# Optimization experiments

Hardware: AMD Instinct MI355X
Metric: run time of the kernel (lower is better)

Reference implementation:

```python
import jax, jax.numpy as jnp
import numpy as np

DIM = 512
HEADS = 8
DIM_HEAD = 64
HIDDEN = HEADS * DIM_HEAD  # 512
SCALE = DIM_HEAD ** -0.5


def setup_inputs() -> dict:
    key = jax.random.key(0)
    k1, k2, k3, k4 = jax.random.split(key, 4)
    B, N = 8, 4096
    x = jax.random.normal(k1, (B, DIM, N), dtype=jnp.float32)
    # Conv1d with kernel_size=1, no bias -> weight [out, in]
    w_qkv = jax.random.normal(k2, (HIDDEN * 3, DIM), dtype=jnp.float32) * (DIM ** -0.5)
    w_out = jax.random.normal(k3, (DIM, HIDDEN), dtype=jnp.float32) * (HIDDEN ** -0.5)
    b_out = jax.random.normal(k4, (DIM,), dtype=jnp.float32) * 0.01
    return {"x": x, "w_qkv": w_qkv, "w_out": w_out, "b_out": b_out}


def reference(x, w_qkv, w_out, b_out):
    B, _, N = x.shape
    # pointwise conv1d == channel GEMM: [3*hidden, dim] x [b, dim, n]
    qkv = jnp.einsum('oi,bin->bon', w_qkv, x)
    q, k, v = jnp.split(qkv, 3, axis=1)
    # b (h c) n -> b h c n
    reshape = lambda t: t.reshape(B, HEADS, DIM_HEAD, N)
    q, k, v = reshape(q), reshape(k), reshape(v)
    q = q * SCALE
    k = jax.nn.softmax(k, axis=-1)  # softmax over sequence dim n
    # context: [b h d e] = sum_n k[b h d n] v[b h e n]
    context = jnp.einsum('bhdn,bhen->bhde', k, v)
    # out: [b h e n] = sum_d context[b h d e] q[b h d n]
    out = jnp.einsum('bhde,bhdn->bhen', context, q)
    out = out.reshape(B, HIDDEN, N)  # b (h e) n
    return jnp.einsum('oi,bin->bon', w_out, out) + b_out[None, :, None]
```

## Files before the change

kernel.cpp:

```cpp
#include <hip/hip_runtime.h>
#include <hip/hip_bf16.h>
#include <cstdint>

typedef unsigned short u16;
typedef __attribute__((ext_vector_type(8))) short bf16x8;
typedef __attribute__((ext_vector_type(4))) float f32x4;

__device__ __forceinline__ u16 f2b(float f) {
  union { float f; unsigned u; } x; x.f = f;
  unsigned r = x.u + 0x7fffu + ((x.u >> 16) & 1u);
  return (u16)(r >> 16);
}
__device__ __forceinline__ float b2f(u16 u) {
  union { unsigned u; float f; } x; x.u = ((unsigned)u) << 16;
  return x.f;
}
__device__ __forceinline__ void gld16(void* lds, const void* g) {
  __builtin_amdgcn_global_load_lds((const __attribute__((address_space(1))) void*)g,
                                   (__attribute__((address_space(3))) void*)lds, 16, 0, 0);
}
__device__ __forceinline__ int sw_idx(int n, int c) {
  return n * 64 + ((((c >> 2) ^ (n >> 2)) & 15) << 2) + (c & 3);
}
__device__ __forceinline__ int ekb(int row, int c2) {
  return (row * 256 + c2) ^ ((((row >> 3) ^ row) & 7) << 4);
}

__global__ __launch_bounds__(256) void prep(const float* __restrict__ w_qkv,
                                            u16* __restrict__ wkvh,
                                            u16* __restrict__ wqT,
                                            float* __restrict__ zbuf) {
  const int tid = threadIdx.x;
  const int blk = blockIdx.x;
  if (blk < 512) {
    const int i = blk * 1024 + tid * 4;
    const int ri = i >> 9;
    const int col = i & 511;
    const int h = (ri >> 6) & 7;
    const int orow = h * 128 + ((ri >> 9) << 6) + (ri & 63);
    const float4 v = *(const float4*)(w_qkv + 262144 + i);
    ushort4 r; r.x = f2b(v.x); r.y = f2b(v.y); r.z = f2b(v.z); r.w = f2b(v.w);
    *(ushort4*)(wkvh + orow * 512 + col) = r;
  } else if (blk < 576) {
    __shared__ u16 t[4096];
    const int bb = blk - 512;
    const int i0 = (bb & 7) * 64;
    const int c0 = (bb >> 3) * 64;
    const int il = (tid & 15) * 4;
    const int cl = tid >> 4;
#pragma unroll
    for (int r = 0; r < 4; r++) {
      const int c = cl + r * 16;
      const float4 v = *(const float4*)(w_qkv + (c0 + c) * 512 + i0 + il);
      t[sw_idx(il + 0, c)] = f2b(v.x);
      t[sw_idx(il + 1, c)] = f2b(v.y);
      t[sw_idx(il + 2, c)] = f2b(v.z);
      t[sw_idx(il + 3, c)] = f2b(v.w);
    }
    __syncthreads();
    const int cw = (tid & 15) * 4;
#pragma unroll
    for (int r = 0; r < 4; r++) {
      const int i = cl + r * 16;
      const u16* tp = &t[sw_idx(i, cw)];
      ushort4 o; o.x = tp[0]; o.y = tp[1]; o.z = tp[2]; o.w = tp[3];
      *(ushort4*)(wqT + (i0 + i) * 512 + c0 + cw) = o;
    }
  } else {
    const int zi = (blk - 576) * 1024 + tid * 4;
    if (zi < 266240) *(float4*)(zbuf + zi) = float4{0.f, 0.f, 0.f, 0.f};
  }
}

__global__ __launch_bounds__(256) void xt_kern(const float* __restrict__ x,
                                               u16* __restrict__ xt) {
  __shared__ u16 t[4096];
  const int tid = threadIdx.x;
  const int b = blockIdx.z;
  const int n0 = blockIdx.x * 64;
  const int c0 = blockIdx.y * 64;
  const int nl = (tid & 15) * 4;
  const int cl = tid >> 4;
#pragma unroll
  for (int r = 0; r < 4; r++) {
    const int c = cl + r * 16;
    const float4 v = *(const float4*)(x + ((long)b * 512 + c0 + c) * 4096 + n0 + nl);
    t[sw_idx(nl + 0, c)] = f2b(v.x);
    t[sw_idx(nl + 1, c)] = f2b(v.y);
    t[sw_idx(nl + 2, c)] = f2b(v.z);
    t[sw_idx(nl + 3, c)] = f2b(v.w);
  }
  __syncthreads();
  const int cw = (tid & 15) * 4;
#pragma unroll
  for (int r = 0; r < 4; r++) {
    const int n = cl + r * 16;
    const u16* tp = &t[sw_idx(n, cw)];
    ushort4 o; o.x = tp[0]; o.y = tp[1]; o.z = tp[2]; o.w = tp[3];
    *(ushort4*)(xt + ((long)b * 4096 + n0 + n) * 512 + c0 + cw) = o;
  }
}

__global__ __launch_bounds__(256, 4) void kvctx(const u16* __restrict__ wkvh,
                                                const u16* __restrict__ xt,
                                                float* __restrict__ ctx,
                                                float* __restrict__ rsum) {
  __shared__ u16 sh[16384];
  u16* As = sh;
  u16* Bs = sh + 4096;
  u16* Ek = sh;
  u16* Vs = sh + 8192;

  const int tid = threadIdx.x;
  const int wid = tid >> 6;
  const int lane = tid & 63;
  const int wm = wid >> 1, wn = wid & 1;

  const int flat = blockIdx.x;
  const int xcd = flat & 7;
  const int slot = flat >> 3;
  const int h = slot & 7;
  const int tile = xcd * 32 + (slot >> 3);
  const int nc = tile & 31;
  const int b = tile >> 5;
  const int bh = b * 8 + h;

  const u16* Ab = wkvh + (long)h * 128 * 512;
  const u16* Bb = xt + ((long)b * 4096 + (long)nc * 128) * 512;
  const int q8 = (lane >> 4) * 8;
  const int mr = lane & 15;
  const int quad = lane >> 4;

  f32x4 acc[4][4] = {};

  for (int kk = 0; kk < 512; kk += 32) {
    __syncthreads();
#pragma unroll
    for (int i = 0; i < 2; i++) {
      const int slot2 = i * 256 + tid;
      const int row = slot2 >> 2;
      const int kc = (slot2 & 3) * 8;
      gld16((char*)As + i * 4096 + wid * 1024, Ab + (long)row * 512 + kk + kc);
      gld16((char*)Bs + i * 4096 + wid * 1024, Bb + (long)row * 512 + kk + kc);
    }
    __syncthreads();
    bf16x8 af[4], bfv[4];
#pragma unroll
    for (int i = 0; i < 4; i++)
      af[i] = *(const bf16x8*)(As + (wm * 64 + i * 16 + mr) * 32 + q8);
#pragma unroll
    for (int j = 0; j < 4; j++)
      bfv[j] = *(const bf16x8*)(Bs + (wn * 64 + j * 16 + mr) * 32 + q8);
#pragma unroll
    for (int i = 0; i < 4; i++)
#pragma unroll
      for (int j = 0; j < 4; j++)
        acc[i][j] = __builtin_amdgcn_mfma_f32_16x16x32_bf16(af[i], bfv[j], acc[i][j], 0, 0, 0);
  }

  __syncthreads();
  u16* dst = (wm == 0) ? Ek : Vs;
#pragma unroll
  for (int i = 0; i < 4; i++) {
#pragma unroll
    for (int r = 0; r < 4; r++) {
      const int row = i * 16 + quad * 4 + r;
      float sloc = 0.f;
#pragma unroll
      for (int j = 0; j < 4; j++) {
        float v = acc[i][j][r];
        if (wm == 0) v = __expf(v);
        const u16 bv = f2b(v);
        const int col = wn * 64 + j * 16 + mr;
        *(u16*)((char*)dst + ekb(row, col * 2)) = bv;
        if (wm == 0) sloc += b2f(bv);
      }
      if (wm == 0) {
        sloc += __shfl_xor(sloc, 1);
        sloc += __shfl_xor(sloc, 2);
        sloc += __shfl_xor(sloc, 4);
        sloc += __shfl_xor(sloc, 8);
        if (mr == 0) atomicAdd(rsum + (long)bh * 64 + row, sloc);
      }
    }
  }
  __syncthreads();

  f32x4 acc2[2][2] = {};
#pragma unroll
  for (int ks = 0; ks < 4; ks++) {
    bf16x8 ef[2], vf[2];
#pragma unroll
    for (int ii = 0; ii < 2; ii++) {
      const int row = wm * 32 + ii * 16 + mr;
      ef[ii] = *(const bf16x8*)((const char*)Ek + ekb(row, (ks * 32 + q8) * 2));
    }
#pragma unroll
    for (int jj = 0; jj < 2; jj++) {
      const int row = wn * 32 + jj * 16 + mr;
      vf[jj] = *(const bf16x8*)((const char*)Vs + ekb(row, (ks * 32 + q8) * 2));
    }
#pragma unroll
    for (int ii = 0; ii < 2; ii++)
#pragma unroll
      for (int jj = 0; jj < 2; jj++)
        acc2[ii][jj] = __builtin_amdgcn_mfma_f32_16x16x32_bf16(ef[ii], vf[jj], acc2[ii][jj], 0, 0, 0);
  }

  float* cb = ctx + (long)bh * 4096;
#pragma unroll
  for (int ii = 0; ii < 2; ii++)
#pragma unroll
    for (int jj = 0; jj < 2; jj++)
#pragma unroll
      for (int r = 0; r < 4; r++) {
        const int d = wm * 32 + ii * 16 + quad * 4 + r;
        const int e = wn * 32 + jj * 16 + mr;
        atomicAdd(cb + d * 64 + e, acc2[ii][jj][r]);
      }
}

__global__ __launch_bounds__(256) void wc_kern(const float* __restrict__ ctxp,
                                               const float* __restrict__ rsump,
                                               const float* __restrict__ wout,
                                               u16* __restrict__ Wc) {
  __shared__ float cs[64 * 65];
  const int tid = threadIdx.x;
  const int bh = blockIdx.x, og = blockIdx.y;
  const int b = bh >> 3, h = bh & 7;
  for (int i = tid; i < 4096; i += 256) {
    const int d = i >> 6, e = i & 63;
    cs[e * 65 + d] = ctxp[(long)bh * 4096 + i] / rsump[(long)bh * 64 + d];
  }
  __syncthreads();
  const int d = tid & 63;
  const int o0 = og * 128 + (tid >> 6) * 32;
  float csr[64];
#pragma unroll
  for (int e = 0; e < 64; e++) csr[e] = cs[e * 65 + d];
  u16* wcp = Wc + (long)b * 512 * 512;
  for (int rr = 0; rr < 32; rr++) {
    const int o = o0 + rr;
    const float* wrow = wout + (long)o * 512 + h * 64;
    float a0 = 0.f, a1 = 0.f, a2 = 0.f, a3 = 0.f;
#pragma unroll
    for (int e = 0; e < 64; e += 4) {
      a0 += wrow[e + 0] * csr[e + 0];
      a1 += wrow[e + 1] * csr[e + 1];
      a2 += wrow[e + 2] * csr[e + 2];
      a3 += wrow[e + 3] * csr[e + 3];
    }
    wcp[(long)o * 512 + h * 64 + d] = f2b((a0 + a1) + (a2 + a3));
  }
}

__global__ __launch_bounds__(256) void weff_gemm(const u16* __restrict__ Wc,
                                                 const u16* __restrict__ wqT,
                                                 u16* __restrict__ Weff) {
  __shared__ u16 As[128 * 32];
  __shared__ u16 Bs[128 * 32];
  const int tid = threadIdx.x;
  const int wid = tid >> 6;
  const int lane = tid & 63;
  const int wm = wid >> 1, wn = wid & 1;
  const int gn = blockIdx.x, gm = blockIdx.y, b = blockIdx.z;

  const u16* Ab = Wc + (long)b * 512 * 512 + (long)gm * 128 * 512;
  const u16* Bb = wqT + (long)gn * 128 * 512;

  f32x4 acc[4][4] = {};
  const int q8 = (lane >> 4) * 8;
  const int mr = lane & 15;

  for (int kk = 0; kk < 512; kk += 32) {
    __syncthreads();
#pragma unroll
    for (int i = 0; i < 2; i++) {
      const int slot = i * 256 + tid;
      const int row = slot >> 2;
      const int kc = (slot & 3) * 8;
      gld16((char*)As + i * 4096 + wid * 1024, Ab + (long)row * 512 + kk + kc);
      gld16((char*)Bs + i * 4096 + wid * 1024, Bb + (long)row * 512 + kk + kc);
    }
    __syncthreads();
    bf16x8 af[4], bfv[4];
#pragma unroll
    for (int i = 0; i < 4; i++)
      af[i] = *(const bf16x8*)(As + (wm * 64 + i * 16 + mr) * 32 + q8);
#pragma unroll
    for (int j = 0; j < 4; j++)
      bfv[j] = *(const bf16x8*)(Bs + (wn * 64 + j * 16 + mr) * 32 + q8);
#pragma unroll
    for (int i = 0; i < 4; i++)
#pragma unroll
      for (int j = 0; j < 4; j++)
        acc[i][j] = __builtin_amdgcn_mfma_f32_16x16x32_bf16(af[i], bfv[j], acc[i][j], 0, 0, 0);
  }

  const int col = lane & 15;
  const int quad = lane >> 4;
  u16* wb = Weff + (long)b * 512 * 512;
#pragma unroll
  for (int i = 0; i < 4; i++)
#pragma unroll
    for (int r = 0; r < 4; r++) {
      const int grow = gm * 128 + wm * 64 + i * 16 + quad * 4 + r;
#pragma unroll
      for (int j = 0; j < 4; j++) {
        const int gcol = gn * 128 + wn * 64 + j * 16 + col;
        wb[(long)grow * 512 + gcol] = f2b(acc[i][j][r] * 0.125f);
      }
    }
}

__global__ __launch_bounds__(256) void out_gemm(const u16* __restrict__ Weff,
                                                const u16* __restrict__ xt,
                                                const float* __restrict__ bias,
                                                float* __restrict__ outp) {
  __shared__ u16 As[128 * 32];
  __shared__ u16 Bs[128 * 32];
  const int tid = threadIdx.x;
  const int wid = tid >> 6;
  const int lane = tid & 63;
  const int wm = wid >> 1, wn = wid & 1;
  const int gn = blockIdx.x, gm = blockIdx.y, b = blockIdx.z;

  const u16* Ab = Weff + (long)b * 512 * 512 + (long)gm * 128 * 512;
  const u16* Bb = xt + ((long)b * 4096 + (long)gn * 128) * 512;

  f32x4 acc[4][4] = {};
  const int q8 = (lane >> 4) * 8;
  const int mr = lane & 15;

  for (int kk = 0; kk < 512; kk += 32) {
    __syncthreads();
#pragma unroll
    for (int i = 0; i < 2; i++) {
      const int slot = i * 256 + tid;
      const int row = slot >> 2;
      const int kc = (slot & 3) * 8;
      gld16((char*)As + i * 4096 + wid * 1024, Ab + (long)row * 512 + kk + kc);
      gld16((char*)Bs + i * 4096 + wid * 1024, Bb + (long)row * 512 + kk + kc);
    }
    __syncthreads();
    bf16x8 af[4], bfv[4];
#pragma unroll
    for (int i = 0; i < 4; i++)
      af[i] = *(const bf16x8*)(As + (wm * 64 + i * 16 + mr) * 32 + q8);
#pragma unroll
    for (int j = 0; j < 4; j++)
      bfv[j] = *(const bf16x8*)(Bs + (wn * 64 + j * 16 + mr) * 32 + q8);
#pragma unroll
    for (int i = 0; i < 4; i++)
#pragma unroll
      for (int j = 0; j < 4; j++)
        acc[i][j] = __builtin_amdgcn_mfma_f32_16x16x32_bf16(af[i], bfv[j], acc[i][j], 0, 0, 0);
  }

  const int col = lane & 15;
  const int quad = lane >> 4;
#pragma unroll
  for (int i = 0; i < 4; i++)
#pragma unroll
    for (int r = 0; r < 4; r++) {
      const int grow = gm * 128 + wm * 64 + i * 16 + quad * 4 + r;
      const float bv = bias[grow];
#pragma unroll
      for (int j = 0; j < 4; j++) {
        const long gcol = (long)gn * 128 + wn * 64 + j * 16 + col;
        outp[((long)b * 512 + grow) * 4096 + gcol] = acc[i][j][r] + bv;
      }
    }
}

extern "C" void kernel_launch(void* const* d_in, const int* in_sizes, int n_in,
                              void* d_out, int out_size, void* d_ws, size_t ws_size,
                              hipStream_t stream) {
  const float* x = (const float*)d_in[0];
  const float* w_qkv = (const float*)d_in[1];
  const float* w_out = (const float*)d_in[2];
  const float* b_out = (const float*)d_in[3];
  float* out = (float*)d_out;
  char* ws = (char*)d_ws;

  u16* xt = (u16*)(ws + 0);
  u16* wkvh = (u16*)(ws + 33554432);
  u16* wqT = (u16*)(ws + 34603008);
  u16* wc = (u16*)(ws + 35127296);
  u16* weff = (u16*)(ws + 39321600);
  float* ctx = (float*)(ws + 43515904);
  float* rsum = (float*)(ws + 44564480);

  prep<<<836, 256, 0, stream>>>(w_qkv, wkvh, wqT, ctx);
  xt_kern<<<dim3(64, 8, 8), 256, 0, stream>>>(x, xt);
  kvctx<<<2048, 256, 0, stream>>>(wkvh, xt, ctx, rsum);
  wc_kern<<<dim3(64, 4), 256, 0, stream>>>(ctx, rsum, w_out, wc);
  weff_gemm<<<dim3(4, 4, 8), 256, 0, stream>>>(wc, wqT, weff);
  out_gemm<<<dim3(32, 4, 8), 256, 0, stream>>>(weff, xt, b_out, out);
}
```

Before: 265.2 us.

## Double-buffer LDS with XOR swizzle in GEMMs and merge prep kernels

The kvctx and out_gemm main loops now use two LDS buffers. The next K-slice's global_load_lds is issued before computing on the current one, so each step needs one barrier instead of two. The LDS column chunks are XOR-swizzled by row so the fragment reads hit fewer bank conflicts. The x transpose kernel is also folded into the weight prep kernel, removing one launch. The cost is double the LDS per block in out_gemm, which may limit occupancy.

```diff
diff --git a/kernel.cpp b/kernel.cpp
--- a/kernel.cpp
+++ b/kernel.cpp
@@ -26,14 +26,44 @@
   return (row * 256 + c2) ^ ((((row >> 3) ^ row) & 7) << 4);
 }
 
-__global__ __launch_bounds__(256) void prep(const float* __restrict__ w_qkv,
-                                            u16* __restrict__ wkvh,
-                                            u16* __restrict__ wqT,
-                                            float* __restrict__ zbuf) {
+__global__ __launch_bounds__(256) void pre(const float* __restrict__ x,
+                                           u16* __restrict__ xt,
+                                           const float* __restrict__ w_qkv,
+                                           u16* __restrict__ wkvh,
+                                           u16* __restrict__ wqT,
+                                           float* __restrict__ zbuf) {
+  __shared__ u16 t[4096];
   const int tid = threadIdx.x;
   const int blk = blockIdx.x;
-  if (blk < 512) {
-    const int i = blk * 1024 + tid * 4;
+  if (blk < 4096) {
+    const int b = blk >> 9;
+    const int c0 = ((blk >> 6) & 7) * 64;
+    const int n0 = (blk & 63) * 64;
+    const int nl = (tid & 15) * 4;
+    const int cl = tid >> 4;
+#pragma unroll
+    for (int r = 0; r < 4; r++) {
+      const int c = cl + r * 16;
+      const float4 v = *(const float4*)(x + ((long)b * 512 + c0 + c) * 4096 + n0 + nl);
+      t[sw_idx(nl + 0, c)] = f2b(v.x);
+      t[sw_idx(nl + 1, c)] = f2b(v.y);
+      t[sw_idx(nl + 2, c)] = f2b(v.z);
+      t[sw_idx(nl + 3, c)] = f2b(v.w);
+    }
+    __syncthreads();
+    const int cw = (tid & 15) * 4;
+#pragma unroll
+    for (int r = 0; r < 4; r++) {
+      const int n = cl + r * 16;
+      const u16* tp = &t[sw_idx(n, cw)];
+      ushort4 o; o.x = tp[0]; o.y = tp[1]; o.z = tp[2]; o.w = tp[3];
+      *(ushort4*)(xt + ((long)b * 4096 + n0 + n) * 512 + c0 + cw) = o;
+    }
+    return;
+  }
+  const int pblk = blk - 4096;
+  if (pblk < 512) {
+    const int i = pblk * 1024 + tid * 4;
     const int ri = i >> 9;
     const int col = i & 511;
     const int h = (ri >> 6) & 7;
@@ -41,9 +71,8 @@
     const float4 v = *(const float4*)(w_qkv + 262144 + i);
     ushort4 r; r.x = f2b(v.x); r.y = f2b(v.y); r.z = f2b(v.z); r.w = f2b(v.w);
     *(ushort4*)(wkvh + orow * 512 + col) = r;
-  } else if (blk < 576) {
-    __shared__ u16 t[4096];
-    const int bb = blk - 512;
+  } else if (pblk < 576) {
+    const int bb = pblk - 512;
     const int i0 = (bb & 7) * 64;
     const int c0 = (bb >> 3) * 64;
     const int il = (tid & 15) * 4;
@@ -67,37 +96,8 @@
       *(ushort4*)(wqT + (i0 + i) * 512 + c0 + cw) = o;
     }
   } else {
-    const int zi = (blk - 576) * 1024 + tid * 4;
+    const int zi = (pblk - 576) * 1024 + tid * 4;
     if (zi < 266240) *(float4*)(zbuf + zi) = float4{0.f, 0.f, 0.f, 0.f};
-  }
-}
-
-__global__ __launch_bounds__(256) void xt_kern(const float* __restrict__ x,
-                                               u16* __restrict__ xt) {
-  __shared__ u16 t[4096];
-  const int tid = threadIdx.x;
-  const int b = blockIdx.z;
-  const int n0 = blockIdx.x * 64;
-  const int c0 = blockIdx.y * 64;
-  const int nl = (tid & 15) * 4;
-  const int cl = tid >> 4;
-#pragma unroll
-  for (int r = 0; r < 4; r++) {
-    const int c = cl + r * 16;
-    const float4 v = *(const float4*)(x + ((long)b * 512 + c0 + c) * 4096 + n0 + nl);
-    t[sw_idx(nl + 0, c)] = f2b(v.x);
-    t[sw_idx(nl + 1, c)] = f2b(v.y);
-    t[sw_idx(nl + 2, c)] = f2b(v.z);
-    t[sw_idx(nl + 3, c)] = f2b(v.w);
-  }
-  __syncthreads();
-  const int cw = (tid & 15) * 4;
-#pragma unroll
-  for (int r = 0; r < 4; r++) {
-    const int n = cl + r * 16;
-    const u16* tp = &t[sw_idx(n, cw)];
-    ushort4 o; o.x = tp[0]; o.y = tp[1]; o.z = tp[2]; o.w = tp[3];
-    *(ushort4*)(xt + ((long)b * 4096 + n0 + n) * 512 + c0 + cw) = o;
   }
 }
 
@@ -106,8 +106,6 @@
                                                 float* __restrict__ ctx,
                                                 float* __restrict__ rsum) {
   __shared__ u16 sh[16384];
-  u16* As = sh;
-  u16* Bs = sh + 4096;
   u16* Ek = sh;
   u16* Vs = sh + 8192;
 
@@ -127,30 +125,38 @@
 
   const u16* Ab = wkvh + (long)h * 128 * 512;
   const u16* Bb = xt + ((long)b * 4096 + (long)nc * 128) * 512;
-  const int q8 = (lane >> 4) * 8;
   const int mr = lane & 15;
   const int quad = lane >> 4;
+  const int q8 = quad * 8;
+  const int cidx = (quad ^ ((mr >> 1) & 3)) * 8;
 
   f32x4 acc[4][4] = {};
 
-  for (int kk = 0; kk < 512; kk += 32) {
-    __syncthreads();
+  auto stage = [&](int buf, int kk) {
 #pragma unroll
     for (int i = 0; i < 2; i++) {
-      const int slot2 = i * 256 + tid;
-      const int row = slot2 >> 2;
-      const int kc = (slot2 & 3) * 8;
-      gld16((char*)As + i * 4096 + wid * 1024, Ab + (long)row * 512 + kk + kc);
-      gld16((char*)Bs + i * 4096 + wid * 1024, Bb + (long)row * 512 + kk + kc);
-    }
-    __syncthreads();
+      const int s2 = i * 256 + tid;
+      const int row = s2 >> 2;
+      const int kc = (((s2 & 3) ^ ((row >> 1) & 3)) * 8);
+      char* dA = (char*)sh + buf * 16384 + i * 4096 + wid * 1024;
+      gld16(dA, Ab + (long)row * 512 + kk + kc);
+      gld16(dA + 8192, Bb + (long)row * 512 + kk + kc);
+    }
+  };
+
+  stage(0, 0);
+  for (int t = 0; t < 16; t++) {
+    __syncthreads();
+    if (t < 15) stage((t + 1) & 1, (t + 1) * 32);
+    const u16* As = sh + (t & 1) * 8192;
+    const u16* Bs = As + 4096;
     bf16x8 af[4], bfv[4];
 #pragma unroll
     for (int i = 0; i < 4; i++)
-      af[i] = *(const bf16x8*)(As + (wm * 64 + i * 16 + mr) * 32 + q8);
+      af[i] = *(const bf16x8*)(As + (wm * 64 + i * 16 + mr) * 32 + cidx);
 #pragma unroll
     for (int j = 0; j < 4; j++)
-      bfv[j] = *(const bf16x8*)(Bs + (wn * 64 + j * 16 + mr) * 32 + q8);
+      bfv[j] = *(const bf16x8*)(Bs + (wn * 64 + j * 16 + mr) * 32 + cidx);
 #pragma unroll
     for (int i = 0; i < 4; i++)
 #pragma unroll
@@ -317,8 +323,7 @@
                                                 const u16* __restrict__ xt,
                                                 const float* __restrict__ bias,
                                                 float* __restrict__ outp) {
-  __shared__ u16 As[128 * 32];
-  __shared__ u16 Bs[128 * 32];
+  __shared__ u16 sh[16384];
   const int tid = threadIdx.x;
   const int wid = tid >> 6;
   const int lane = tid & 63;
@@ -329,27 +334,35 @@
   const u16* Bb = xt + ((long)b * 4096 + (long)gn * 128) * 512;
 
   f32x4 acc[4][4] = {};
-  const int q8 = (lane >> 4) * 8;
   const int mr = lane & 15;
-
-  for (int kk = 0; kk < 512; kk += 32) {
-    __syncthreads();
+  const int quad = lane >> 4;
+  const int cidx = (quad ^ ((mr >> 1) & 3)) * 8;
+
+  auto stage = [&](int buf, int kk) {
 #pragma unroll
     for (int i = 0; i < 2; i++) {
-      const int slot = i * 256 + tid;
-      const int row = slot >> 2;
-      const int kc = (slot & 3) * 8;
-      gld16((char*)As + i * 4096 + wid * 1024, Ab + (long)row * 512 + kk + kc);
-      gld16((char*)Bs + i * 4096 + wid * 1024, Bb + (long)row * 512 + kk + kc);
-    }
-    __syncthreads();
+      const int s2 = i * 256 + tid;
+      const int row = s2 >> 2;
+      const int kc = (((s2 & 3) ^ ((row >> 1) & 3)) * 8);
+      char* dA = (char*)sh + buf * 16384 + i * 4096 + wid * 1024;
+      gld16(dA, Ab + (long)row * 512 + kk + kc);
+      gld16(dA + 8192, Bb + (long)row * 512 + kk + kc);
+    }
+  };
+
+  stage(0, 0);
+  for (int t = 0; t < 16; t++) {
+    __syncthreads();
+    if (t < 15) stage((t + 1) & 1, (t + 1) * 32);
+    const u16* As = sh + (t & 1) * 8192;
+    const u16* Bs = As + 4096;
     bf16x8 af[4], bfv[4];
 #pragma unroll
     for (int i = 0; i < 4; i++)
-      af[i] = *(const bf16x8*)(As + (wm * 64 + i * 16 + mr) * 32 + q8);
+      af[i] = *(const bf16x8*)(As + (wm * 64 + i * 16 + mr) * 32 + cidx);
 #pragma unroll
     for (int j = 0; j < 4; j++)
-      bfv[j] = *(const bf16x8*)(Bs + (wn * 64 + j * 16 + mr) * 32 + q8);
+      bfv[j] = *(const bf16x8*)(Bs + (wn * 64 + j * 16 + mr) * 32 + cidx);
 #pragma unroll
     for (int i = 0; i < 4; i++)
 #pragma unroll
@@ -358,7 +371,6 @@
   }
 
   const int col = lane & 15;
-  const int quad = lane >> 4;
 #pragma unroll
   for (int i = 0; i < 4; i++)
 #pragma unroll
@@ -391,8 +403,7 @@
   float* ctx = (float*)(ws + 43515904);
   float* rsum = (float*)(ws + 44564480);
 
-  prep<<<836, 256, 0, stream>>>(w_qkv, wkvh, wqT, ctx);
-  xt_kern<<<dim3(64, 8, 8), 256, 0, stream>>>(x, xt);
+  pre<<<4932, 256, 0, stream>>>(x, xt, w_qkv, wkvh, wqT, ctx);
   kvctx<<<2048, 256, 0, stream>>>(wkvh, xt, ctx, rsum);
   wc_kern<<<dim3(64, 4), 256, 0, stream>>>(ctx, rsum, w_out, wc);
   weff_gemm<<<dim3(4, 4, 8), 256, 0, stream>>>(wc, wqT, weff);
```

After: 258.4 us. 1.03x faster.
